# Optimization experiments

Measured on AMD Instinct MI355X. Metric: run time of the kernel, lower is better.

## Reference

```python
import jax, jax.numpy as jnp
import numpy as np
import math

B, N, D_MODEL = 1, 2925, 1536
NUM_HEADS, HEAD_DIM = 12, 128
F, H, W = 13, 15, 15
MAX_SEQ = 1024
EPS = 1e-6


def _make_freqs(max_seq, dim):
    # (cos, sin) pairs for half-dim rotary frequencies, base 10000
    inv = 1.0 / (10000.0 ** (np.arange(0, dim, 2, dtype=np.float64) / dim))
    ang = np.arange(max_seq, dtype=np.float64)[:, None] * inv[None, :]
    return jnp.asarray(np.stack([np.cos(ang), np.sin(ang)], axis=-1), dtype=jnp.float32)


def setup_inputs() -> dict:
    key = jax.random.key(0)
    ks = jax.random.split(key, 10)
    s = 1.0 / math.sqrt(D_MODEL)
    dim_base = HEAD_DIM // 6              # 21
    dim_t = HEAD_DIM - 4 * dim_base       # 44
    dim_h = 2 * dim_base                  # 42
    return {
        "x": jax.random.normal(ks[0], (B, N, D_MODEL), dtype=jnp.float32),
        "Wq": jax.random.normal(ks[1], (D_MODEL, D_MODEL), dtype=jnp.float32) * s,
        "bq": jnp.zeros((D_MODEL,), dtype=jnp.float32),
        "Wk": jax.random.normal(ks[2], (D_MODEL, D_MODEL), dtype=jnp.float32) * s,
        "bk": jnp.zeros((D_MODEL,), dtype=jnp.float32),
        "Wv": jax.random.normal(ks[3], (D_MODEL, D_MODEL), dtype=jnp.float32) * s,
        "bv": jnp.zeros((D_MODEL,), dtype=jnp.float32),
        "Wo": jax.random.normal(ks[4], (D_MODEL, D_MODEL), dtype=jnp.float32) * s,
        "bo": jnp.zeros((D_MODEL,), dtype=jnp.float32),
        "q_scale": jnp.ones((D_MODEL,), dtype=jnp.float32),
        "k_scale": jnp.ones((D_MODEL,), dtype=jnp.float32),
        "freqs_t": _make_freqs(MAX_SEQ, dim_t),
        "freqs_h": _make_freqs(MAX_SEQ, dim_h),
        "freqs_w": _make_freqs(MAX_SEQ, dim_h),
        "f": F, "h": H, "w": W,
    }


def _rms_norm(x, scale, eps=EPS):
    var = jnp.mean(jnp.square(x), axis=-1, keepdims=True)
    return x * jax.lax.rsqrt(var + eps) * scale


def _rope_apply(x, f, h, w, freqs_t, freqs_h, freqs_w):
    # x: [b, n, H, D] with n == f*h*w
    b, n, nh, d = x.shape
    db = d // 6
    dt, dh, dw = d - 4 * db, 2 * db, 2 * db
    ft = jnp.broadcast_to(freqs_t[:f, None, None, :, :], (f, h, w, dt // 2, 2))
    fh = jnp.broadcast_to(freqs_h[None, :h, None, :, :], (f, h, w, dh // 2, 2))
    fw = jnp.broadcast_to(freqs_w[None, None, :w, :, :], (f, h, w, dw // 2, 2))
    fg = jnp.concatenate([ft, fh, fw], axis=3).reshape(n, d // 2, 2)[None, :, None, :, :]
    xc = x.reshape(b, n, nh, d // 2, 2)
    re = xc[..., 0] * fg[..., 0] - xc[..., 1] * fg[..., 1]
    im = xc[..., 0] * fg[..., 1] + xc[..., 1] * fg[..., 0]
    return jnp.stack([re, im], axis=-1).reshape(b, n, nh, d)


def reference(x, Wq, bq, Wk, bk, Wv, bv, Wo, bo, q_scale, k_scale,
              freqs_t, freqs_h, freqs_w, f, h, w):
    b, n, _ = x.shape
    nh, d = NUM_HEADS, HEAD_DIM
    # projections + RMSNorm across full hidden dim (before head split)
    q = _rms_norm(x @ Wq + bq, q_scale).reshape(b, n, nh, d)
    k = _rms_norm(x @ Wk + bk, k_scale).reshape(b, n, nh, d)
    v = (x @ Wv + bv).reshape(b, n, nh, d)
    # 3D RoPE on [b, n, H, D] layout
    q = _rope_apply(q, f, h, w, freqs_t, freqs_h, freqs_w)
    k = _rope_apply(k, f, h, w, freqs_t, freqs_h, freqs_w)
    # [b, H, n, d]
    q = q.transpose(0, 2, 1, 3)
    k = k.transpose(0, 2, 1, 3)
    v = v.transpose(0, 2, 1, 3)
    scores = jnp.einsum("bhid,bhjd->bhij", q, k) / math.sqrt(d)
    attn = jax.nn.softmax(scores, axis=-1)
    out = jnp.einsum("bhij,bhjd->bhid", attn, v)
    out = out.transpose(0, 2, 1, 3).reshape(b, n, nh * d)
    return out @ Wo + bo
```

## Files before the change

kernel.cpp:

```cpp
#include <hip/hip_runtime.h>


#define N_TOK 2925
#define DMODEL 1536
#define NHEAD 12
#define HDIM 128
#define KSPLIT 1472
#define VT_STRIDE 2944

typedef __attribute__((ext_vector_type(8))) __bf16 bf16x8;
typedef __attribute__((ext_vector_type(4))) float floatx4;

#define MFMA(a, b, c) __builtin_amdgcn_mfma_f32_16x16x32_bf16((a), (b), (c), 0, 0, 0)

static __device__ __forceinline__ unsigned short f2bf(float f) {
    unsigned u = __builtin_bit_cast(unsigned, f);
    return (unsigned short)((u + 0x7fffu + ((u >> 16) & 1u)) >> 16);
}

static __device__ __forceinline__ void gload_lds16(const unsigned short* g, unsigned short* l) {
    __builtin_amdgcn_global_load_lds((const __attribute__((address_space(1))) void*)g,
                                     (__attribute__((address_space(3))) void*)l, 16, 0, 0);
}

__global__ __launch_bounds__(256) void k_convert_x(const float* __restrict__ x,
                                                   unsigned short* __restrict__ xb, int n) {
    int i = (blockIdx.x * 256 + threadIdx.x) * 4;
    if (i < n) {
        float4 v = *(const float4*)(x + i);
        uint2 o;
        o.x = (unsigned)f2bf(v.x) | ((unsigned)f2bf(v.y) << 16);
        o.y = (unsigned)f2bf(v.z) | ((unsigned)f2bf(v.w) << 16);
        *(uint2*)(xb + i) = o;
    }
}

__global__ __launch_bounds__(256) void k_transpose_w(const float* __restrict__ W0,
                                                     const float* __restrict__ W1,
                                                     const float* __restrict__ W2,
                                                     const float* __restrict__ W3,
                                                     unsigned short* __restrict__ Wt) {
    __shared__ float tile[32][33];
    const float* W = blockIdx.z == 0 ? W0 : blockIdx.z == 1 ? W1 : blockIdx.z == 2 ? W2 : W3;
    unsigned short* out = Wt + (size_t)blockIdx.z * DMODEL * DMODEL;
    int tx = threadIdx.x, ty = threadIdx.y;
    int bx = blockIdx.x * 32, by = blockIdx.y * 32;
#pragma unroll
    for (int i = 0; i < 4; i++)
        tile[ty + 8 * i][tx] = W[(size_t)(by + ty + 8 * i) * DMODEL + bx + tx];
    __syncthreads();
#pragma unroll
    for (int i = 0; i < 4; i++)
        out[(size_t)(bx + ty + 8 * i) * DMODEL + by + tx] = f2bf(tile[tx][ty + 8 * i]);
}

__global__ __launch_bounds__(256, 2) void k_gemm(const unsigned short* __restrict__ A,
                                                 const unsigned short* __restrict__ BtBase,
                                                 const float* __restrict__ b0,
                                                 const float* __restrict__ b1,
                                                 const float* __restrict__ b2,
                                                 float* __restrict__ Cbase, int M) {
    const int z = blockIdx.z;
    const unsigned short* Bt = BtBase + (size_t)z * DMODEL * DMODEL;
    const float* bias = (z == 0) ? b0 : (z == 1) ? b1 : b2;
    float* C = Cbase + (size_t)z * M * DMODEL;

    __shared__ __align__(16) unsigned short As[128 * 32];
    __shared__ __align__(16) unsigned short Bs[128 * 32];

    const int tid = threadIdx.x;
    const int wave = tid >> 6, lane = tid & 63, quad = lane >> 4, l16 = lane & 15;
    const int wr = wave >> 1, wc = wave & 1;
    const int m0 = blockIdx.y * 128, n0 = blockIdx.x * 128;

    const int r4 = tid >> 2, c4 = (tid & 3) * 8;

    floatx4 acc[4][4] = {};

    for (int k0 = 0; k0 < DMODEL; k0 += 32) {
        gload_lds16(A + (size_t)(m0 + r4) * DMODEL + k0 + c4,       &As[r4 * 32 + c4]);
        gload_lds16(A + (size_t)(m0 + r4 + 64) * DMODEL + k0 + c4,  &As[(r4 + 64) * 32 + c4]);
        gload_lds16(Bt + (size_t)(n0 + r4) * DMODEL + k0 + c4,      &Bs[r4 * 32 + c4]);
        gload_lds16(Bt + (size_t)(n0 + r4 + 64) * DMODEL + k0 + c4, &Bs[(r4 + 64) * 32 + c4]);
        __syncthreads();

        bf16x8 af[4], bfm[4];
#pragma unroll
        for (int i = 0; i < 4; i++)
            af[i] = *(const bf16x8*)&As[(wr * 64 + i * 16 + l16) * 32 + quad * 8];
#pragma unroll
        for (int j = 0; j < 4; j++)
            bfm[j] = *(const bf16x8*)&Bs[(wc * 64 + j * 16 + l16) * 32 + quad * 8];
#pragma unroll
        for (int i = 0; i < 4; i++)
#pragma unroll
            for (int j = 0; j < 4; j++)
                acc[i][j] = MFMA(af[i], bfm[j], acc[i][j]);
        __syncthreads();
    }

#pragma unroll
    for (int j = 0; j < 4; j++) {
        int cg = n0 + wc * 64 + j * 16 + l16;
        float bv = bias[cg];
#pragma unroll
        for (int i = 0; i < 4; i++) {
            int rbase = m0 + wr * 64 + i * 16 + quad * 4;
#pragma unroll
            for (int r = 0; r < 4; r++) {
                int rg = rbase + r;
                if (rg < M) C[(size_t)rg * DMODEL + cg] = acc[i][j][r] + bv;
            }
        }
    }
}

__global__ __launch_bounds__(256) void k_norm_rope(const float* __restrict__ Qf,
                                                   const float* __restrict__ Kf,
                                                   const float* __restrict__ Vf,
                                                   const float* __restrict__ qsc,
                                                   const float* __restrict__ ksc,
                                                   const float* __restrict__ ft,
                                                   const float* __restrict__ fh,
                                                   const float* __restrict__ fw,
                                                   unsigned short* __restrict__ qb,
                                                   unsigned short* __restrict__ kb,
                                                   unsigned short* __restrict__ vb) {
    const int n = blockIdx.x;
    const int tid = threadIdx.x, wave = tid >> 6, lane = tid & 63;
    const int t_i = n / 225, rem = n % 225, h_i = rem / 15, w_i = rem % 15;
    const float att_scale = 0.08838834764831845f * 1.4426950408889634f;

    float2 qv[3], kv[3], vv[3];
    float sq = 0.f, sk = 0.f;
#pragma unroll
    for (int c = 0; c < 3; c++) {
        int p = tid + 256 * c;
        qv[c] = *(const float2*)(Qf + (size_t)n * DMODEL + 2 * p);
        kv[c] = *(const float2*)(Kf + (size_t)n * DMODEL + 2 * p);
        vv[c] = *(const float2*)(Vf + (size_t)n * DMODEL + 2 * p);
        sq += qv[c].x * qv[c].x + qv[c].y * qv[c].y;
        sk += kv[c].x * kv[c].x + kv[c].y * kv[c].y;
    }
#pragma unroll
    for (int off = 32; off >= 1; off >>= 1) {
        sq += __shfl_xor(sq, off, 64);
        sk += __shfl_xor(sk, off, 64);
    }
    __shared__ float red[2][4];
    if (lane == 0) { red[0][wave] = sq; red[1][wave] = sk; }
    __syncthreads();
    sq = red[0][0] + red[0][1] + red[0][2] + red[0][3];
    sk = red[1][0] + red[1][1] + red[1][2] + red[1][3];
    const float rq = rsqrtf(sq * (1.f / 1536.f) + 1e-6f) * att_scale;
    const float rk = rsqrtf(sk * (1.f / 1536.f) + 1e-6f);

#pragma unroll
    for (int c = 0; c < 3; c++) {
        int p = tid + 256 * c;
        int hd = p >> 6, pl = p & 63, dd = 2 * pl;
        float cs, sn;
        if (pl < 22)      { cs = ft[t_i * 44 + 2 * pl];        sn = ft[t_i * 44 + 2 * pl + 1]; }
        else if (pl < 43) { int pp = pl - 22; cs = fh[h_i * 42 + 2 * pp]; sn = fh[h_i * 42 + 2 * pp + 1]; }
        else              { int pp = pl - 43; cs = fw[w_i * 42 + 2 * pp]; sn = fw[w_i * 42 + 2 * pp + 1]; }
        int hidx = hd * 128 + dd;
        float q0 = qv[c].x * rq * qsc[hidx], q1 = qv[c].y * rq * qsc[hidx + 1];
        float k0 = kv[c].x * rk * ksc[hidx], k1 = kv[c].y * rk * ksc[hidx + 1];
        size_t o = ((size_t)hd * N_TOK + n) * HDIM + dd;
        unsigned qo = (unsigned)f2bf(q0 * cs - q1 * sn) | ((unsigned)f2bf(q0 * sn + q1 * cs) << 16);
        unsigned ko = (unsigned)f2bf(k0 * cs - k1 * sn) | ((unsigned)f2bf(k0 * sn + k1 * cs) << 16);
        unsigned vo = (unsigned)f2bf(vv[c].x) | ((unsigned)f2bf(vv[c].y) << 16);
        *(unsigned*)(qb + o) = qo;
        *(unsigned*)(kb + o) = ko;
        *(unsigned*)(vb + o) = vo;
    }
}

__global__ __launch_bounds__(256) void k_transpose_v(const unsigned short* __restrict__ vbi,
                                                     unsigned short* __restrict__ vt) {
    __shared__ unsigned short tile[32][33];
    const int head = blockIdx.z;
    const int t0 = blockIdx.x * 32, d0 = blockIdx.y * 32;
    const int tx = threadIdx.x, ty = threadIdx.y;
#pragma unroll
    for (int i = 0; i < 4; i++) {
        int t = t0 + ty + 8 * i;
        tile[ty + 8 * i][tx] = (t < N_TOK) ? vbi[((size_t)head * N_TOK + t) * HDIM + d0 + tx] : 0;
    }
    __syncthreads();
    int t = t0 + tx;
#pragma unroll
    for (int i = 0; i < 4; i++)
        vt[((size_t)head * HDIM + d0 + ty + 8 * i) * VT_STRIDE + t] = tile[tx][ty + 8 * i];
}

__global__ __launch_bounds__(256, 3) void k_attn_part(const unsigned short* __restrict__ qb,
                                                      const unsigned short* __restrict__ kb,
                                                      const unsigned short* __restrict__ vt,
                                                      float* __restrict__ Opart,
                                                      float* __restrict__ mbuf,
                                                      float* __restrict__ lbuf) {
    __shared__ unsigned short Ks[64 * 136];
    __shared__ unsigned short Vs[128 * 72];
    __shared__ unsigned short Ps[4][16 * 72];

    const int tid = threadIdx.x, wave = tid >> 6, lane = tid & 63;
    const int quad = lane >> 4, l16 = lane & 15;
    const int head = blockIdx.y, z = blockIdx.z;
    const int q0 = blockIdx.x * 64 + wave * 16;
    const unsigned short* qh = qb + (size_t)head * N_TOK * HDIM;
    const unsigned short* kh = kb + (size_t)head * N_TOK * HDIM;
    const unsigned short* vh = vt + (size_t)head * HDIM * VT_STRIDE;
    unsigned short* ps = Ps[wave];

    const int kbeg = z ? KSPLIT : 0;
    const int kend = z ? N_TOK : KSPLIT;

    bf16x8 aq[4];
    {
        int qrow = q0 + l16;
        if (qrow < N_TOK) {
#pragma unroll
            for (int ks = 0; ks < 4; ks++)
                aq[ks] = *(const bf16x8*)&qh[(size_t)qrow * HDIM + ks * 32 + quad * 8];
        } else {
#pragma unroll
            for (int ks = 0; ks < 4; ks++) aq[ks] = (bf16x8)(__bf16)0.0f;
        }
    }

    floatx4 oacc[8] = {};
    float m_r[4] = {-1e30f, -1e30f, -1e30f, -1e30f};
    float l_r[4] = {0.f, 0.f, 0.f, 0.f};

    for (int kb0 = kbeg; kb0 < kend; kb0 += 64) {
#pragma unroll
        for (int c = 0; c < 4; c++) {
            int chunk = tid + 256 * c;
            int row = chunk >> 4, col = (chunk & 15) * 8;
            int gk = kb0 + row; if (gk >= N_TOK) gk = N_TOK - 1;
            *(uint4*)&Ks[row * 136 + col] = *(const uint4*)(kh + (size_t)gk * HDIM + col);
        }
#pragma unroll
        for (int c = 0; c < 4; c++) {
            int chunk = tid + 256 * c;
            int d = chunk >> 3, col = (chunk & 7) * 8;
            *(uint4*)&Vs[d * 72 + col] = *(const uint4*)(vh + (size_t)d * VT_STRIDE + kb0 + col);
        }
        __syncthreads();

        floatx4 sa[4] = {};
#pragma unroll
        for (int j = 0; j < 4; j++) {
            bf16x8 bkf[4];
#pragma unroll
            for (int ks = 0; ks < 4; ks++)
                bkf[ks] = *(const bf16x8*)&Ks[(j * 16 + l16) * 136 + ks * 32 + quad * 8];
#pragma unroll
            for (int ks = 0; ks < 4; ks++)
                sa[j] = MFMA(aq[ks], bkf[ks], sa[j]);
        }

        bool valid[4];
#pragma unroll
        for (int j = 0; j < 4; j++) valid[j] = (kb0 + j * 16 + l16) < kend;

        float alpha[4];
#pragma unroll
        for (int r = 0; r < 4; r++) {
            float x = -1e30f;
#pragma unroll
            for (int j = 0; j < 4; j++) x = fmaxf(x, valid[j] ? sa[j][r] : -1e30f);
#pragma unroll
            for (int off = 8; off >= 1; off >>= 1) x = fmaxf(x, __shfl_xor(x, off, 16));
            float mnew = fmaxf(m_r[r], x);
            alpha[r] = exp2f(m_r[r] - mnew);
            m_r[r] = mnew;
        }
        float rsum[4] = {0.f, 0.f, 0.f, 0.f};
#pragma unroll
        for (int j = 0; j < 4; j++)
#pragma unroll
            for (int r = 0; r < 4; r++) {
                float p = valid[j] ? exp2f(sa[j][r] - m_r[r]) : 0.f;
                rsum[r] += p;
                ps[(quad * 4 + r) * 72 + j * 16 + l16] = f2bf(p);
            }
#pragma unroll
        for (int r = 0; r < 4; r++) {
            float s = rsum[r];
#pragma unroll
            for (int off = 8; off >= 1; off >>= 1) s += __shfl_xor(s, off, 16);
            l_r[r] = l_r[r] * alpha[r] + s;
        }
#pragma unroll
        for (int jd = 0; jd < 8; jd++)
#pragma unroll
            for (int r = 0; r < 4; r++) oacc[jd][r] *= alpha[r];

#pragma unroll
        for (int ks = 0; ks < 2; ks++) {
            bf16x8 ap = *(const bf16x8*)&ps[l16 * 72 + ks * 32 + quad * 8];
#pragma unroll
            for (int jd = 0; jd < 8; jd++) {
                bf16x8 bvf = *(const bf16x8*)&Vs[(jd * 16 + l16) * 72 + ks * 32 + quad * 8];
                oacc[jd] = MFMA(ap, bvf, oacc[jd]);
            }
        }
        __syncthreads();
    }

#pragma unroll
    for (int r = 0; r < 4; r++) {
        int rg = q0 + quad * 4 + r;
        if (rg < N_TOK) {
            size_t rbase = ((size_t)(z * NHEAD + head) * N_TOK + rg) * HDIM;
#pragma unroll
            for (int jd = 0; jd < 8; jd++)
                Opart[rbase + jd * 16 + l16] = oacc[jd][r];
            if (l16 == 0) {
                int mi = (z * NHEAD + head) * N_TOK + rg;
                mbuf[mi] = m_r[r];
                lbuf[mi] = l_r[r];
            }
        }
    }
}

__global__ __launch_bounds__(256) void k_combine(const float* __restrict__ Opart,
                                                 const float* __restrict__ mbuf,
                                                 const float* __restrict__ lbuf,
                                                 unsigned short* __restrict__ ab) {
    const int R = NHEAD * N_TOK;
    int r = blockIdx.x * 8 + (threadIdx.x >> 5);
    if (r >= R) return;
    int l32 = threadIdx.x & 31;
    float m0 = mbuf[r], m1 = mbuf[R + r];
    float l0 = lbuf[r], l1 = lbuf[R + r];
    float m = fmaxf(m0, m1);
    float w0 = exp2f(m0 - m), w1 = exp2f(m1 - m);
    float inv = 1.f / (l0 * w0 + l1 * w1);
    w0 *= inv; w1 *= inv;
    float4 a = *(const float4*)&Opart[(size_t)r * HDIM + l32 * 4];
    float4 b = *(const float4*)&Opart[((size_t)R + r) * HDIM + l32 * 4];
    int head = r / N_TOK, tok = r % N_TOK;
    unsigned short* o = ab + (size_t)tok * DMODEL + head * HDIM + l32 * 4;
    uint2 pk;
    pk.x = (unsigned)f2bf(a.x * w0 + b.x * w1) | ((unsigned)f2bf(a.y * w0 + b.y * w1) << 16);
    pk.y = (unsigned)f2bf(a.z * w0 + b.z * w1) | ((unsigned)f2bf(a.w * w0 + b.w * w1) << 16);
    *(uint2*)o = pk;
}

extern "C" void kernel_launch(void* const* d_in, const int* in_sizes, int n_in,
                              void* d_out, int out_size, void* d_ws, size_t ws_size,
                              hipStream_t stream) {
    const float* x   = (const float*)d_in[0];
    const float* Wq  = (const float*)d_in[1];
    const float* bq  = (const float*)d_in[2];
    const float* Wk  = (const float*)d_in[3];
    const float* bk  = (const float*)d_in[4];
    const float* Wv  = (const float*)d_in[5];
    const float* bv  = (const float*)d_in[6];
    const float* Wo  = (const float*)d_in[7];
    const float* bo  = (const float*)d_in[8];
    const float* qsc = (const float*)d_in[9];
    const float* ksc = (const float*)d_in[10];
    const float* ft  = (const float*)d_in[11];
    const float* fh  = (const float*)d_in[12];
    const float* fw  = (const float*)d_in[13];

    char* ws = (char*)d_ws;
    unsigned short* xb   = (unsigned short*)ws; ws += (size_t)N_TOK * DMODEL * 2;
    unsigned short* Wt   = (unsigned short*)ws; ws += (size_t)4 * DMODEL * DMODEL * 2;
    unsigned short* ab   = (unsigned short*)ws; ws += (size_t)N_TOK * DMODEL * 2;
    char* qkvf_region    = ws;                  ws += (size_t)3 * N_TOK * DMODEL * 4;
    unsigned short* qkvb = (unsigned short*)ws; ws += (size_t)3 * N_TOK * DMODEL * 2;

    float* Qf = (float*)qkvf_region;
    float* Kf = Qf + (size_t)N_TOK * DMODEL;
    float* Vf = Qf + (size_t)2 * N_TOK * DMODEL;
    float* Opart = (float*)qkvf_region;
    float* mbuf  = Opart + (size_t)2 * NHEAD * N_TOK * HDIM;
    float* lbuf  = mbuf + (size_t)2 * NHEAD * N_TOK;
    unsigned short* vtp = (unsigned short*)(lbuf + (size_t)2 * NHEAD * N_TOK);

    unsigned short* qbp = qkvb;
    unsigned short* kbp = qkvb + (size_t)N_TOK * DMODEL;
    unsigned short* vbp = qkvb + (size_t)2 * N_TOK * DMODEL;

    const int nelem = N_TOK * DMODEL;
    k_convert_x<<<(nelem / 4 + 255) / 256, 256, 0, stream>>>(x, xb, nelem);
    k_transpose_w<<<dim3(48, 48, 4), dim3(32, 8), 0, stream>>>(Wq, Wk, Wv, Wo, Wt);
    k_gemm<<<dim3(12, 23, 3), 256, 0, stream>>>(xb, Wt, bq, bk, bv, Qf, N_TOK);
    k_norm_rope<<<N_TOK, 256, 0, stream>>>(Qf, Kf, Vf, qsc, ksc, ft, fh, fw, qbp, kbp, vbp);
    k_transpose_v<<<dim3(92, 4, NHEAD), dim3(32, 8), 0, stream>>>(vbp, vtp);
    k_attn_part<<<dim3(46, NHEAD, 2), 256, 0, stream>>>(qbp, kbp, vtp, Opart, mbuf, lbuf);
    k_combine<<<(NHEAD * N_TOK + 7) / 8, 256, 0, stream>>>(Opart, mbuf, lbuf, ab);
    k_gemm<<<dim3(12, 23, 1), 256, 0, stream>>>(ab, Wt + (size_t)3 * DMODEL * DMODEL,
                                                bo, bo, bo, (float*)d_out, N_TOK);
}
```

Measured before the change: 423.6 us.

## Transpose attention MFMA operands so each lane owns one query row

Swaps the A/B operands of both attention MFMAs so the accumulator holds S^T and O^T, putting one query row in each lane's 16-lane column. Softmax max and sum then need one scalar per lane and two cross-quad shuffles, replacing four rows with four-step 16-lane butterflies. P is packed to bf16 with a truncating byte-permute and written as 8-byte stores, and outputs are written as float4. The truncating bf16 conversion drops round-to-nearest, which slightly changes numerics.

```diff
diff --git a/kernel.cpp b/kernel.cpp
--- a/kernel.cpp
+++ b/kernel.cpp
@@ -16,6 +16,10 @@
 static __device__ __forceinline__ unsigned short f2bf(float f) {
     unsigned u = __builtin_bit_cast(unsigned, f);
     return (unsigned short)((u + 0x7fffu + ((u >> 16) & 1u)) >> 16);
+}
+static __device__ __forceinline__ unsigned packbf2(float a, float b) {
+    return __builtin_amdgcn_perm(__builtin_bit_cast(unsigned, b),
+                                 __builtin_bit_cast(unsigned, a), 0x07060302u);
 }
 
 static __device__ __forceinline__ void gload_lds16(const unsigned short* g, unsigned short* l) {
@@ -230,8 +234,7 @@
     }
 
     floatx4 oacc[8] = {};
-    float m_r[4] = {-1e30f, -1e30f, -1e30f, -1e30f};
-    float l_r[4] = {0.f, 0.f, 0.f, 0.f};
+    float m_r = -1e30f, l_r = 0.f;
 
     for (int kb0 = kbeg; kb0 < kend; kb0 += 64) {
 #pragma unroll
@@ -252,51 +255,46 @@
         floatx4 sa[4] = {};
 #pragma unroll
         for (int j = 0; j < 4; j++) {
-            bf16x8 bkf[4];
-#pragma unroll
-            for (int ks = 0; ks < 4; ks++)
-                bkf[ks] = *(const bf16x8*)&Ks[(j * 16 + l16) * 136 + ks * 32 + quad * 8];
-#pragma unroll
-            for (int ks = 0; ks < 4; ks++)
-                sa[j] = MFMA(aq[ks], bkf[ks], sa[j]);
-        }
-
-        bool valid[4];
-#pragma unroll
-        for (int j = 0; j < 4; j++) valid[j] = (kb0 + j * 16 + l16) < kend;
-
-        float alpha[4];
-#pragma unroll
-        for (int r = 0; r < 4; r++) {
-            float x = -1e30f;
-#pragma unroll
-            for (int j = 0; j < 4; j++) x = fmaxf(x, valid[j] ? sa[j][r] : -1e30f);
-#pragma unroll
-            for (int off = 8; off >= 1; off >>= 1) x = fmaxf(x, __shfl_xor(x, off, 16));
-            float mnew = fmaxf(m_r[r], x);
-            alpha[r] = exp2f(m_r[r] - mnew);
-            m_r[r] = mnew;
-        }
-        float rsum[4] = {0.f, 0.f, 0.f, 0.f};
+#pragma unroll
+            for (int ks = 0; ks < 4; ks++) {
+                bf16x8 bk = *(const bf16x8*)&Ks[(j * 16 + l16) * 136 + ks * 32 + quad * 8];
+                sa[j] = MFMA(bk, aq[ks], sa[j]);
+            }
+        }
+
+        const int krel = kend - kb0;
+        float mnew = m_r;
 #pragma unroll
         for (int j = 0; j < 4; j++)
 #pragma unroll
             for (int r = 0; r < 4; r++) {
-                float p = valid[j] ? exp2f(sa[j][r] - m_r[r]) : 0.f;
-                rsum[r] += p;
-                ps[(quad * 4 + r) * 72 + j * 16 + l16] = f2bf(p);
-            }
-#pragma unroll
-        for (int r = 0; r < 4; r++) {
-            float s = rsum[r];
-#pragma unroll
-            for (int off = 8; off >= 1; off >>= 1) s += __shfl_xor(s, off, 16);
-            l_r[r] = l_r[r] * alpha[r] + s;
-        }
+                if (j * 16 + quad * 4 + r >= krel) sa[j][r] = -1e30f;
+                mnew = fmaxf(mnew, sa[j][r]);
+            }
+        mnew = fmaxf(mnew, __shfl_xor(mnew, 16, 64));
+        mnew = fmaxf(mnew, __shfl_xor(mnew, 32, 64));
+        const float alpha = exp2f(m_r - mnew);
+        m_r = mnew;
+
+        float rsum = 0.f;
+#pragma unroll
+        for (int j = 0; j < 4; j++) {
+            float p0 = exp2f(sa[j][0] - mnew), p1 = exp2f(sa[j][1] - mnew);
+            float p2 = exp2f(sa[j][2] - mnew), p3 = exp2f(sa[j][3] - mnew);
+            rsum += (p0 + p1) + (p2 + p3);
+            uint2 pk;
+            pk.x = packbf2(p0, p1);
+            pk.y = packbf2(p2, p3);
+            *(uint2*)&ps[l16 * 72 + j * 16 + quad * 4] = pk;
+        }
+        rsum += __shfl_xor(rsum, 16, 64);
+        rsum += __shfl_xor(rsum, 32, 64);
+        l_r = l_r * alpha + rsum;
+
 #pragma unroll
         for (int jd = 0; jd < 8; jd++)
 #pragma unroll
-            for (int r = 0; r < 4; r++) oacc[jd][r] *= alpha[r];
+            for (int r = 0; r < 4; r++) oacc[jd][r] *= alpha;
 
 #pragma unroll
         for (int ks = 0; ks < 2; ks++) {
@@ -304,24 +302,24 @@
 #pragma unroll
             for (int jd = 0; jd < 8; jd++) {
                 bf16x8 bvf = *(const bf16x8*)&Vs[(jd * 16 + l16) * 72 + ks * 32 + quad * 8];
-                oacc[jd] = MFMA(ap, bvf, oacc[jd]);
+                oacc[jd] = MFMA(bvf, ap, oacc[jd]);
             }
         }
         __syncthreads();
     }
 
-#pragma unroll
-    for (int r = 0; r < 4; r++) {
-        int rg = q0 + quad * 4 + r;
-        if (rg < N_TOK) {
-            size_t rbase = ((size_t)(z * NHEAD + head) * N_TOK + rg) * HDIM;
+    {
+        int qrow = q0 + l16;
+        if (qrow < N_TOK) {
+            size_t rbase = ((size_t)(z * NHEAD + head) * N_TOK + qrow) * HDIM;
 #pragma unroll
             for (int jd = 0; jd < 8; jd++)
-                Opart[rbase + jd * 16 + l16] = oacc[jd][r];
-            if (l16 == 0) {
-                int mi = (z * NHEAD + head) * N_TOK + rg;
-                mbuf[mi] = m_r[r];
-                lbuf[mi] = l_r[r];
+                *(float4*)&Opart[rbase + jd * 16 + quad * 4] =
+                    *(const float4*)&oacc[jd];
+            if (quad == 0) {
+                int mi = (z * NHEAD + head) * N_TOK + qrow;
+                mbuf[mi] = m_r;
+                lbuf[mi] = l_r;
             }
         }
     }
```

After: 448.7 us. 1.06x slower.

## Process two query tiles per wave, split keys four ways, store bf16 partials

Applied to the files above, without the earlier changes.

Each wave now handles 32 query rows instead of 16, so every K/V tile loaded into LDS feeds twice as many MFMAs. The key range is split into four chunks instead of two, which keeps the grid size roughly the same (23x12x4 blocks). Partial outputs are stored as bf16 rather than fp32, halving the partial-buffer traffic into the combine kernel. In exchange, register pressure rises under launch bounds of 3 blocks per CU, there is extra rounding in the partials, and there is a redundant mbuf write loop (later overwritten by the correct one).

```diff
diff --git a/kernel.cpp b/kernel.cpp
--- a/kernel.cpp
+++ b/kernel.cpp
@@ -5,8 +5,8 @@
 #define DMODEL 1536
 #define NHEAD 12
 #define HDIM 128
-#define KSPLIT 1472
 #define VT_STRIDE 2944
+#define NSPLIT 4
 
 typedef __attribute__((ext_vector_type(8))) __bf16 bf16x8;
 typedef __attribute__((ext_vector_type(4))) float floatx4;
@@ -16,6 +16,10 @@
 static __device__ __forceinline__ unsigned short f2bf(float f) {
     unsigned u = __builtin_bit_cast(unsigned, f);
     return (unsigned short)((u + 0x7fffu + ((u >> 16) & 1u)) >> 16);
+}
+static __device__ __forceinline__ float bf2f(unsigned short s) {
+    unsigned u = ((unsigned)s) << 16;
+    return __builtin_bit_cast(float, u);
 }
 
 static __device__ __forceinline__ void gload_lds16(const unsigned short* g, unsigned short* l) {
@@ -197,41 +201,41 @@
 __global__ __launch_bounds__(256, 3) void k_attn_part(const unsigned short* __restrict__ qb,
                                                       const unsigned short* __restrict__ kb,
                                                       const unsigned short* __restrict__ vt,
-                                                      float* __restrict__ Opart,
+                                                      unsigned short* __restrict__ Opart,
                                                       float* __restrict__ mbuf,
                                                       float* __restrict__ lbuf) {
     __shared__ unsigned short Ks[64 * 136];
     __shared__ unsigned short Vs[128 * 72];
-    __shared__ unsigned short Ps[4][16 * 72];
+    __shared__ unsigned short Ps[4][32 * 72];
 
     const int tid = threadIdx.x, wave = tid >> 6, lane = tid & 63;
     const int quad = lane >> 4, l16 = lane & 15;
     const int head = blockIdx.y, z = blockIdx.z;
-    const int q0 = blockIdx.x * 64 + wave * 16;
+    const int kbeg = (z <= 2) ? z * 768 : 2240;
+    const int kend = (z <= 1) ? (z + 1) * 768 : (z == 2 ? 2240 : N_TOK);
+    const int q0 = blockIdx.x * 128 + wave * 32;
     const unsigned short* qh = qb + (size_t)head * N_TOK * HDIM;
     const unsigned short* kh = kb + (size_t)head * N_TOK * HDIM;
     const unsigned short* vh = vt + (size_t)head * HDIM * VT_STRIDE;
     unsigned short* ps = Ps[wave];
 
-    const int kbeg = z ? KSPLIT : 0;
-    const int kend = z ? N_TOK : KSPLIT;
-
-    bf16x8 aq[4];
-    {
-        int qrow = q0 + l16;
+    bf16x8 aq[2][4];
+#pragma unroll
+    for (int g = 0; g < 2; g++) {
+        int qrow = q0 + g * 16 + l16;
         if (qrow < N_TOK) {
 #pragma unroll
             for (int ks = 0; ks < 4; ks++)
-                aq[ks] = *(const bf16x8*)&qh[(size_t)qrow * HDIM + ks * 32 + quad * 8];
+                aq[g][ks] = *(const bf16x8*)&qh[(size_t)qrow * HDIM + ks * 32 + quad * 8];
         } else {
 #pragma unroll
-            for (int ks = 0; ks < 4; ks++) aq[ks] = (bf16x8)(__bf16)0.0f;
-        }
-    }
-
-    floatx4 oacc[8] = {};
-    float m_r[4] = {-1e30f, -1e30f, -1e30f, -1e30f};
-    float l_r[4] = {0.f, 0.f, 0.f, 0.f};
+            for (int ks = 0; ks < 4; ks++) aq[g][ks] = (bf16x8)(__bf16)0.0f;
+        }
+    }
+
+    floatx4 oacc[2][8] = {};
+    float m_r[2][4] = {{-1e30f, -1e30f, -1e30f, -1e30f}, {-1e30f, -1e30f, -1e30f, -1e30f}};
+    float l_r[2][4] = {};
 
     for (int kb0 = kbeg; kb0 < kend; kb0 += 64) {
 #pragma unroll
@@ -249,7 +253,7 @@
         }
         __syncthreads();
 
-        floatx4 sa[4] = {};
+        floatx4 sa[2][4] = {};
 #pragma unroll
         for (int j = 0; j < 4; j++) {
             bf16x8 bkf[4];
@@ -257,77 +261,103 @@
             for (int ks = 0; ks < 4; ks++)
                 bkf[ks] = *(const bf16x8*)&Ks[(j * 16 + l16) * 136 + ks * 32 + quad * 8];
 #pragma unroll
-            for (int ks = 0; ks < 4; ks++)
-                sa[j] = MFMA(aq[ks], bkf[ks], sa[j]);
+            for (int ks = 0; ks < 4; ks++) {
+                sa[0][j] = MFMA(aq[0][ks], bkf[ks], sa[0][j]);
+                sa[1][j] = MFMA(aq[1][ks], bkf[ks], sa[1][j]);
+            }
         }
 
         bool valid[4];
 #pragma unroll
         for (int j = 0; j < 4; j++) valid[j] = (kb0 + j * 16 + l16) < kend;
 
-        float alpha[4];
-#pragma unroll
-        for (int r = 0; r < 4; r++) {
-            float x = -1e30f;
-#pragma unroll
-            for (int j = 0; j < 4; j++) x = fmaxf(x, valid[j] ? sa[j][r] : -1e30f);
-#pragma unroll
-            for (int off = 8; off >= 1; off >>= 1) x = fmaxf(x, __shfl_xor(x, off, 16));
-            float mnew = fmaxf(m_r[r], x);
-            alpha[r] = exp2f(m_r[r] - mnew);
-            m_r[r] = mnew;
-        }
-        float rsum[4] = {0.f, 0.f, 0.f, 0.f};
-#pragma unroll
-        for (int j = 0; j < 4; j++)
+#pragma unroll
+        for (int g = 0; g < 2; g++) {
+            float alpha[4];
 #pragma unroll
             for (int r = 0; r < 4; r++) {
-                float p = valid[j] ? exp2f(sa[j][r] - m_r[r]) : 0.f;
-                rsum[r] += p;
-                ps[(quad * 4 + r) * 72 + j * 16 + l16] = f2bf(p);
-            }
-#pragma unroll
-        for (int r = 0; r < 4; r++) {
-            float s = rsum[r];
-#pragma unroll
-            for (int off = 8; off >= 1; off >>= 1) s += __shfl_xor(s, off, 16);
-            l_r[r] = l_r[r] * alpha[r] + s;
-        }
-#pragma unroll
-        for (int jd = 0; jd < 8; jd++)
-#pragma unroll
-            for (int r = 0; r < 4; r++) oacc[jd][r] *= alpha[r];
+                float x = -1e30f;
+#pragma unroll
+                for (int j = 0; j < 4; j++) x = fmaxf(x, valid[j] ? sa[g][j][r] : -1e30f);
+#pragma unroll
+                for (int off = 8; off >= 1; off >>= 1) x = fmaxf(x, __shfl_xor(x, off, 16));
+                float mnew = fmaxf(m_r[g][r], x);
+                alpha[r] = exp2f(m_r[g][r] - mnew);
+                m_r[g][r] = mnew;
+            }
+            float rsum[4] = {0.f, 0.f, 0.f, 0.f};
+#pragma unroll
+            for (int j = 0; j < 4; j++)
+#pragma unroll
+                for (int r = 0; r < 4; r++) {
+                    float p = valid[j] ? exp2f(sa[g][j][r] - m_r[g][r]) : 0.f;
+                    rsum[r] += p;
+                    ps[(g * 16 + quad * 4 + r) * 72 + j * 16 + l16] = f2bf(p);
+                }
+#pragma unroll
+            for (int r = 0; r < 4; r++) {
+                float s = rsum[r];
+#pragma unroll
+                for (int off = 8; off >= 1; off >>= 1) s += __shfl_xor(s, off, 16);
+                l_r[g][r] = l_r[g][r] * alpha[r] + s;
+            }
+#pragma unroll
+            for (int jd = 0; jd < 8; jd++)
+#pragma unroll
+                for (int r = 0; r < 4; r++) oacc[g][jd][r] *= alpha[r];
+        }
 
 #pragma unroll
         for (int ks = 0; ks < 2; ks++) {
-            bf16x8 ap = *(const bf16x8*)&ps[l16 * 72 + ks * 32 + quad * 8];
+            bf16x8 ap0 = *(const bf16x8*)&ps[l16 * 72 + ks * 32 + quad * 8];
+            bf16x8 ap1 = *(const bf16x8*)&ps[(16 + l16) * 72 + ks * 32 + quad * 8];
 #pragma unroll
             for (int jd = 0; jd < 8; jd++) {
                 bf16x8 bvf = *(const bf16x8*)&Vs[(jd * 16 + l16) * 72 + ks * 32 + quad * 8];
-                oacc[jd] = MFMA(ap, bvf, oacc[jd]);
+                oacc[0][jd] = MFMA(ap0, bvf, oacc[0][jd]);
+                oacc[1][jd] = MFMA(ap1, bvf, oacc[1][jd]);
             }
         }
         __syncthreads();
     }
 
-#pragma unroll
-    for (int r = 0; r < 4; r++) {
-        int rg = q0 + quad * 4 + r;
-        if (rg < N_TOK) {
-            size_t rbase = ((size_t)(z * NHEAD + head) * N_TOK + rg) * HDIM;
-#pragma unroll
-            for (int jd = 0; jd < 8; jd++)
-                Opart[rbase + jd * 16 + l16] = oacc[jd][r];
-            if (l16 == 0) {
-                int mi = (z * NHEAD + head) * N_TOK + rg;
-                mbuf[mi] = m_r[r];
-                lbuf[mi] = l_r[r];
-            }
-        }
-    }
-}
-
-__global__ __launch_bounds__(256) void k_combine(const float* __restrict__ Opart,
+    unsigned short* ob = Opart + (size_t)(z * NHEAD + head) * N_TOK * HDIM;
+#pragma unroll
+    for (int g = 0; g < 2; g++) {
+#pragma unroll
+        for (int r = 0; r < 4; r++) {
+            int rg = q0 + g * 16 + quad * 4 + r;
+            if (rg < N_TOK) {
+#pragma unroll
+                for (int jd = 0; jd < 8; jd++)
+                    ob[(size_t)rg * HDIM + jd * 16 + l16] = f2bf(oacc[g][jd][r]);
+            }
+        }
+        if (quad == 0) {
+            int rg2 = q0 + g * 16 + l16;
+            if (rg2 < N_TOK) {
+                int mi = (z * NHEAD + head) * N_TOK + rg2;
+                mbuf[mi] = m_r[g][l16 & 3];
+            }
+        }
+    }
+#pragma unroll
+    for (int g = 0; g < 2; g++) {
+        if (l16 == 0) {
+#pragma unroll
+            for (int r = 0; r < 4; r++) {
+                int rg = q0 + g * 16 + quad * 4 + r;
+                if (rg < N_TOK) {
+                    int mi = (z * NHEAD + head) * N_TOK + rg;
+                    mbuf[mi] = m_r[g][r];
+                    lbuf[mi] = l_r[g][r];
+                }
+            }
+        }
+    }
+}
+
+__global__ __launch_bounds__(256) void k_combine(const unsigned short* __restrict__ Opart,
                                                  const float* __restrict__ mbuf,
                                                  const float* __restrict__ lbuf,
                                                  unsigned short* __restrict__ ab) {
@@ -335,20 +365,32 @@
     int r = blockIdx.x * 8 + (threadIdx.x >> 5);
     if (r >= R) return;
     int l32 = threadIdx.x & 31;
-    float m0 = mbuf[r], m1 = mbuf[R + r];
-    float l0 = lbuf[r], l1 = lbuf[R + r];
-    float m = fmaxf(m0, m1);
-    float w0 = exp2f(m0 - m), w1 = exp2f(m1 - m);
-    float inv = 1.f / (l0 * w0 + l1 * w1);
-    w0 *= inv; w1 *= inv;
-    float4 a = *(const float4*)&Opart[(size_t)r * HDIM + l32 * 4];
-    float4 b = *(const float4*)&Opart[((size_t)R + r) * HDIM + l32 * 4];
+
+    float m[NSPLIT], l[NSPLIT], w[NSPLIT];
+#pragma unroll
+    for (int s = 0; s < NSPLIT; s++) { m[s] = mbuf[s * R + r]; l[s] = lbuf[s * R + r]; }
+    float mm = fmaxf(fmaxf(m[0], m[1]), fmaxf(m[2], m[3]));
+    float den = 0.f;
+#pragma unroll
+    for (int s = 0; s < NSPLIT; s++) { w[s] = exp2f(m[s] - mm); den += l[s] * w[s]; }
+    float inv = 1.f / den;
+#pragma unroll
+    for (int s = 0; s < NSPLIT; s++) w[s] *= inv;
+
+    float acc[4] = {0.f, 0.f, 0.f, 0.f};
+#pragma unroll
+    for (int s = 0; s < NSPLIT; s++) {
+        uint2 d = *(const uint2*)&Opart[((size_t)s * R + r) * HDIM + l32 * 4];
+        acc[0] += bf2f((unsigned short)(d.x & 0xffff)) * w[s];
+        acc[1] += bf2f((unsigned short)(d.x >> 16)) * w[s];
+        acc[2] += bf2f((unsigned short)(d.y & 0xffff)) * w[s];
+        acc[3] += bf2f((unsigned short)(d.y >> 16)) * w[s];
+    }
     int head = r / N_TOK, tok = r % N_TOK;
-    unsigned short* o = ab + (size_t)tok * DMODEL + head * HDIM + l32 * 4;
     uint2 pk;
-    pk.x = (unsigned)f2bf(a.x * w0 + b.x * w1) | ((unsigned)f2bf(a.y * w0 + b.y * w1) << 16);
-    pk.y = (unsigned)f2bf(a.z * w0 + b.z * w1) | ((unsigned)f2bf(a.w * w0 + b.w * w1) << 16);
-    *(uint2*)o = pk;
+    pk.x = (unsigned)f2bf(acc[0]) | ((unsigned)f2bf(acc[1]) << 16);
+    pk.y = (unsigned)f2bf(acc[2]) | ((unsigned)f2bf(acc[3]) << 16);
+    *(uint2*)(ab + (size_t)tok * DMODEL + head * HDIM + l32 * 4) = pk;
 }
 
 extern "C" void kernel_launch(void* const* d_in, const int* in_sizes, int n_in,
@@ -379,10 +421,10 @@
     float* Qf = (float*)qkvf_region;
     float* Kf = Qf + (size_t)N_TOK * DMODEL;
     float* Vf = Qf + (size_t)2 * N_TOK * DMODEL;
-    float* Opart = (float*)qkvf_region;
-    float* mbuf  = Opart + (size_t)2 * NHEAD * N_TOK * HDIM;
-    float* lbuf  = mbuf + (size_t)2 * NHEAD * N_TOK;
-    unsigned short* vtp = (unsigned short*)(lbuf + (size_t)2 * NHEAD * N_TOK);
+    unsigned short* Opart = (unsigned short*)qkvf_region;
+    float* mbuf = (float*)(qkvf_region + (size_t)NSPLIT * NHEAD * N_TOK * HDIM * 2);
+    float* lbuf = mbuf + (size_t)NSPLIT * NHEAD * N_TOK;
+    unsigned short* vtp = (unsigned short*)(lbuf + (size_t)NSPLIT * NHEAD * N_TOK);
 
     unsigned short* qbp = qkvb;
     unsigned short* kbp = qkvb + (size_t)N_TOK * DMODEL;
@@ -394,7 +436,7 @@
     k_gemm<<<dim3(12, 23, 3), 256, 0, stream>>>(xb, Wt, bq, bk, bv, Qf, N_TOK);
     k_norm_rope<<<N_TOK, 256, 0, stream>>>(Qf, Kf, Vf, qsc, ksc, ft, fh, fw, qbp, kbp, vbp);
     k_transpose_v<<<dim3(92, 4, NHEAD), dim3(32, 8), 0, stream>>>(vbp, vtp);
-    k_attn_part<<<dim3(46, NHEAD, 2), 256, 0, stream>>>(qbp, kbp, vtp, Opart, mbuf, lbuf);
+    k_attn_part<<<dim3(23, NHEAD, NSPLIT), 256, 0, stream>>>(qbp, kbp, vtp, Opart, mbuf, lbuf);
     k_combine<<<(NHEAD * N_TOK + 7) / 8, 256, 0, stream>>>(Opart, mbuf, lbuf, ab);
     k_gemm<<<dim3(12, 23, 1), 256, 0, stream>>>(ab, Wt + (size_t)3 * DMODEL * DMODEL,
                                                 bo, bo, bo, (float*)d_out, N_TOK);
```

New measurement: 529.8 us. 1.25x slower.
